# Kernel optimization log

Measured on AMD Instinct MI355X. Metric: run time of the kernel, lower is better.

## Reference

```python
import jax, jax.numpy as jnp
import numpy as np
from functools import partial

NUM_STEPS = 30  # Euler integration steps (inte_steps)


def _point_sample(vol, pts):
    """Trilinear sample of vol [C,D,H,W] at pts [N,3] (voxel coords, (d,h,w) order).
    Matches torch grid_sample(mode='bilinear', padding_mode='border', align_corners=True)
    after the normalize+flip done in PointPooling. Returns [C,N]."""
    dims = jnp.asarray(vol.shape[1:], dtype=pts.dtype)  # (D,H,W)
    p = jnp.clip(pts, 0.0, dims - 1.0)  # border padding == clamp coords
    p0 = jnp.floor(p)
    frac = p - p0  # [N,3]
    i0 = p0.astype(jnp.int32)
    i1 = jnp.minimum(i0 + 1, (dims - 1.0).astype(jnp.int32))
    d0, h0, w0 = i0[:, 0], i0[:, 1], i0[:, 2]
    d1, h1, w1 = i1[:, 0], i1[:, 1], i1[:, 2]
    fd, fh, fw = frac[:, 0], frac[:, 1], frac[:, 2]
    g = lambda d, h, w: vol[:, d, h, w]  # [C,N] gather
    c000, c001 = g(d0, h0, w0), g(d0, h0, w1)
    c010, c011 = g(d0, h1, w0), g(d0, h1, w1)
    c100, c101 = g(d1, h0, w0), g(d1, h0, w1)
    c110, c111 = g(d1, h1, w0), g(d1, h1, w1)
    c00 = c000 * (1 - fw) + c001 * fw
    c01 = c010 * (1 - fw) + c011 * fw
    c10 = c100 * (1 - fw) + c101 * fw
    c11 = c110 * (1 - fw) + c111 * fw
    c0 = c00 * (1 - fh) + c01 * fh
    c1 = c10 * (1 - fh) + c11 * fh
    return c0 * (1 - fd) + c1 * fd  # [C,N]


def _interp(flow, x):
    # flow [B,3,D,H,W], x [B,N,3] -> [B,N,3]
    out = jax.vmap(_point_sample)(flow, x)  # [B,3,N]
    return jnp.transpose(out, (0, 2, 1))


def _integrate_euler(flow, x, num_steps):
    flow = flow * (1.0 / num_steps)
    def step(x, _):
        return x + _interp(flow, x), None
    x, _ = jax.lax.scan(step, x, None, length=num_steps)
    return x


def _forward(verts, affine, flow_field):
    B, N, _ = verts.shape
    ones = jnp.ones((B, N, 1), dtype=verts.dtype)
    homog = jnp.concatenate([verts, ones], axis=-1)  # [B,N,4]
    pred = jnp.einsum('bij,bnj->bni', affine, homog)[..., :3]
    aux = _integrate_euler(flow_field, pred, NUM_STEPS)
    flow_int = aux - pred  # [B,N,3]
    pred = aux
    flow_int = jnp.transpose(flow_int, (0, 2, 1))[..., None, None]  # [B,3,N,1,1]
    homog2 = jnp.concatenate([pred, ones], axis=-1)
    inv_aff = jnp.linalg.inv(affine)
    pred = jnp.einsum('bij,bnj->bni', inv_aff, homog2)[..., :3]
    return pred, flow_int


def setup_inputs() -> dict:
    key = jax.random.key(0)
    k1, k2, k3 = jax.random.split(key, 3)
    B, N = 2, 140000
    D = H = W = 192
    dims = jnp.asarray([D - 1, H - 1, W - 1], dtype=jnp.float32)
    verts = jax.random.uniform(k1, (B, N, 3), dtype=jnp.float32) * dims
    affine = jnp.eye(4, dtype=jnp.float32)[None] + 0.01 * jax.random.normal(k2, (B, 4, 4), dtype=jnp.float32)
    flow_field = jax.random.normal(k3, (B, 3, D, H, W), dtype=jnp.float32)
    return {"verts": verts, "affine": affine, "flow_field": flow_field}


def reference(verts, affine, flow_field):
    return _forward(verts, affine, flow_field)
```

## Files before the change

kernel.cpp:

```cpp
#include <hip/hip_runtime.h>
#include <hip/hip_fp16.h>

#define NSTEPS 30
#define DIM 192
static constexpr long DHW = (long)DIM * DIM * DIM;
static constexpr int PTS_PER_WAVE = 21;

__global__ void invert4x4_kernel(const float* __restrict__ aff,
                                 float* __restrict__ out, int B) {
    int b = blockIdx.x * blockDim.x + threadIdx.x;
    if (b >= B) return;
    double a[16];
#pragma unroll
    for (int i = 0; i < 16; i++) a[i] = (double)aff[b * 16 + i];
    double s0 = a[0]*a[5]  - a[4]*a[1];
    double s1 = a[0]*a[6]  - a[4]*a[2];
    double s2 = a[0]*a[7]  - a[4]*a[3];
    double s3 = a[1]*a[6]  - a[5]*a[2];
    double s4 = a[1]*a[7]  - a[5]*a[3];
    double s5 = a[2]*a[7]  - a[6]*a[3];
    double c5 = a[10]*a[15] - a[14]*a[11];
    double c4 = a[9]*a[15]  - a[13]*a[11];
    double c3 = a[9]*a[14]  - a[13]*a[10];
    double c2 = a[8]*a[15]  - a[12]*a[11];
    double c1 = a[8]*a[14]  - a[12]*a[10];
    double c0 = a[8]*a[13]  - a[12]*a[9];
    double det = s0*c5 - s1*c4 + s2*c3 + s3*c2 - s4*c1 + s5*c0;
    double inv = 1.0 / det;
    double o[16];
    o[0]  = ( a[5]*c5 - a[6]*c4 + a[7]*c3) * inv;
    o[1]  = (-a[1]*c5 + a[2]*c4 - a[3]*c3) * inv;
    o[2]  = ( a[13]*s5 - a[14]*s4 + a[15]*s3) * inv;
    o[3]  = (-a[9]*s5 + a[10]*s4 - a[11]*s3) * inv;
    o[4]  = (-a[4]*c5 + a[6]*c2 - a[7]*c1) * inv;
    o[5]  = ( a[0]*c5 - a[2]*c2 + a[3]*c1) * inv;
    o[6]  = (-a[12]*s5 + a[14]*s2 - a[15]*s1) * inv;
    o[7]  = ( a[8]*s5 - a[10]*s2 + a[11]*s1) * inv;
    o[8]  = ( a[4]*c4 - a[5]*c2 + a[7]*c0) * inv;
    o[9]  = (-a[0]*c4 + a[1]*c2 - a[3]*c0) * inv;
    o[10] = ( a[12]*s4 - a[13]*s2 + a[15]*s0) * inv;
    o[11] = (-a[8]*s4 + a[9]*s2 - a[11]*s0) * inv;
    o[12] = (-a[4]*c3 + a[5]*c1 - a[6]*c0) * inv;
    o[13] = ( a[0]*c3 - a[1]*c1 + a[2]*c0) * inv;
    o[14] = (-a[12]*s3 + a[13]*s1 - a[14]*s0) * inv;
    o[15] = ( a[8]*s3 - a[9]*s1 + a[10]*s0) * inv;
#pragma unroll
    for (int i = 0; i < 16; i++) out[b * 16 + i] = (float)o[i];
}

__global__ __launch_bounds__(256) void repack_kernel(const float* __restrict__ flow,
                                                     __half* __restrict__ packed) {
    long vox = (long)blockIdx.x * blockDim.x + threadIdx.x;
    int b = blockIdx.y;
    if (vox >= DHW) return;
    const float* F = flow + (size_t)b * 3 * DHW;
    float f0 = F[vox];
    float f1 = F[vox + DHW];
    float f2 = F[vox + 2 * DHW];
    union { __half2 h2[2]; int2 i2; } u;
    u.h2[0] = __floats2half2_rn(f0, f1);
    u.h2[1] = __floats2half2_rn(f2, 0.0f);
    reinterpret_cast<int2*>(packed)[(size_t)b * DHW + vox] = u.i2;
}

__global__ __launch_bounds__(256) void deform_packed_kernel(
    const float* __restrict__ verts,
    const float* __restrict__ affine,
    const __half* __restrict__ packed,
    const float* __restrict__ invaff,
    float* __restrict__ out_pred,
    float* __restrict__ out_flow,
    int N, int B) {
    int lane = threadIdx.x & 63;
    int wib  = threadIdx.x >> 6;
    long gwave = (long)blockIdx.x * (blockDim.x >> 6) + wib;

    int piw = lane / 3;
    if (piw > PTS_PER_WAVE - 1) piw = PTS_PER_WAVE - 1;
    int ch = lane - piw * 3;
    if (ch > 2) ch = 2;

    long pt = gwave * PTS_PER_WAVE + piw;
    bool valid = (lane < 63) && (pt < (long)B * N);
    long ptc = valid ? pt : ((long)B * N - 1);
    int b = (int)(ptc / N);
    int n = (int)(ptc - (long)b * N);

    const float* A = affine + b * 16;
    const float* v = verts + (size_t)ptc * 3;
    float vx = v[0], vy = v[1], vz = v[2];
    float x = A[0] * vx + A[1] * vy + A[2]  * vz + A[3];
    float y = A[4] * vx + A[5] * vy + A[6]  * vz + A[7];
    float z = A[8] * vx + A[9] * vy + A[10] * vz + A[11];
    float p0 = (ch == 0) ? x : (ch == 1) ? y : z;

    const __half* Pb = packed + ((size_t)b * DHW) * 4 + ch;
    const float scale = (float)(1.0 / NSTEPS);

    float cc[8];
    int key = -1;
    int bl = piw * 3;

    for (int s = 0; s < NSTEPS; s++) {
        float pd = fminf(fmaxf(x, 0.0f), (float)(DIM - 1));
        float ph = fminf(fmaxf(y, 0.0f), (float)(DIM - 1));
        float pw = fminf(fmaxf(z, 0.0f), (float)(DIM - 1));
        float fd0 = floorf(pd), fh0 = floorf(ph), fw0 = floorf(pw);
        int d0 = (int)fd0, h0 = (int)fh0, w0 = (int)fw0;
        float fd = pd - fd0, fh = ph - fh0, fw = pw - fw0;

        int k = (d0 * DIM + h0) * DIM + w0;
        if (k != key) {
            key = k;
            int d1 = min(d0 + 1, DIM - 1);
            int h1 = min(h0 + 1, DIM - 1);
            int w1 = min(w0 + 1, DIM - 1);
            size_t r00 = (size_t)((d0 * DIM + h0) * DIM) * 4;
            size_t r01 = (size_t)((d0 * DIM + h1) * DIM) * 4;
            size_t r10 = (size_t)((d1 * DIM + h0) * DIM) * 4;
            size_t r11 = (size_t)((d1 * DIM + h1) * DIM) * 4;
            size_t o0 = (size_t)w0 * 4, o1 = (size_t)w1 * 4;
            cc[0] = __half2float(Pb[r00 + o0]) * scale;
            cc[1] = __half2float(Pb[r00 + o1]) * scale;
            cc[2] = __half2float(Pb[r01 + o0]) * scale;
            cc[3] = __half2float(Pb[r01 + o1]) * scale;
            cc[4] = __half2float(Pb[r10 + o0]) * scale;
            cc[5] = __half2float(Pb[r10 + o1]) * scale;
            cc[6] = __half2float(Pb[r11 + o0]) * scale;
            cc[7] = __half2float(Pb[r11 + o1]) * scale;
        }

        float omfw = 1.0f - fw, omfh = 1.0f - fh, omfd = 1.0f - fd;
        float c00 = cc[0] * omfw + cc[1] * fw;
        float c01 = cc[2] * omfw + cc[3] * fw;
        float c10 = cc[4] * omfw + cc[5] * fw;
        float c11 = cc[6] * omfw + cc[7] * fw;
        float c0 = c00 * omfh + c01 * fh;
        float c1 = c10 * omfh + c11 * fh;
        float val = c0 * omfd + c1 * fd;

        float v0 = __shfl(val, bl,     64);
        float v1 = __shfl(val, bl + 1, 64);
        float v2 = __shfl(val, bl + 2, 64);
        x += v0; y += v1; z += v2;
    }

    if (valid) {
        float posc = (ch == 0) ? x : (ch == 1) ? y : z;
        float fint = posc - p0;
        const float* Ai = invaff + b * 16 + ch * 4;
        float o = Ai[0] * x + Ai[1] * y + Ai[2] * z + Ai[3];
        out_pred[(size_t)ptc * 3 + ch] = o;
        out_flow[(size_t)b * 3 * N + (size_t)ch * N + n] = fint;
    }
}

__global__ __launch_bounds__(256) void deform_kernel(
    const float* __restrict__ verts,
    const float* __restrict__ affine,
    const float* __restrict__ flow,
    const float* __restrict__ invaff,
    float* __restrict__ out_pred,
    float* __restrict__ out_flow,
    int N, int B) {
    int lane = threadIdx.x & 63;
    int wib  = threadIdx.x >> 6;
    long gwave = (long)blockIdx.x * (blockDim.x >> 6) + wib;
    int piw = lane / 3;
    if (piw > PTS_PER_WAVE - 1) piw = PTS_PER_WAVE - 1;
    int ch = lane - piw * 3;
    if (ch > 2) ch = 2;
    long pt = gwave * PTS_PER_WAVE + piw;
    bool valid = (lane < 63) && (pt < (long)B * N);
    long ptc = valid ? pt : ((long)B * N - 1);
    int b = (int)(ptc / N);
    int n = (int)(ptc - (long)b * N);
    const float* A = affine + b * 16;
    const float* v = verts + (size_t)ptc * 3;
    float vx = v[0], vy = v[1], vz = v[2];
    float x = A[0] * vx + A[1] * vy + A[2]  * vz + A[3];
    float y = A[4] * vx + A[5] * vy + A[6]  * vz + A[7];
    float z = A[8] * vx + A[9] * vy + A[10] * vz + A[11];
    float p0 = (ch == 0) ? x : (ch == 1) ? y : z;
    const float* Fc = flow + ((size_t)b * 3 + ch) * (size_t)DHW;
    const float scale = (float)(1.0 / NSTEPS);
    float cc[8];
    int key = -1;
    int bl = piw * 3;
    for (int s = 0; s < NSTEPS; s++) {
        float pd = fminf(fmaxf(x, 0.0f), (float)(DIM - 1));
        float ph = fminf(fmaxf(y, 0.0f), (float)(DIM - 1));
        float pw = fminf(fmaxf(z, 0.0f), (float)(DIM - 1));
        float fd0 = floorf(pd), fh0 = floorf(ph), fw0 = floorf(pw);
        int d0 = (int)fd0, h0 = (int)fh0, w0 = (int)fw0;
        float fd = pd - fd0, fh = ph - fh0, fw = pw - fw0;
        int k = (d0 * DIM + h0) * DIM + w0;
        if (k != key) {
            key = k;
            int d1 = min(d0 + 1, DIM - 1);
            int h1 = min(h0 + 1, DIM - 1);
            int w1 = min(w0 + 1, DIM - 1);
            int r00 = (d0 * DIM + h0) * DIM;
            int r01 = (d0 * DIM + h1) * DIM;
            int r10 = (d1 * DIM + h0) * DIM;
            int r11 = (d1 * DIM + h1) * DIM;
            cc[0] = Fc[r00 + w0] * scale;
            cc[1] = Fc[r00 + w1] * scale;
            cc[2] = Fc[r01 + w0] * scale;
            cc[3] = Fc[r01 + w1] * scale;
            cc[4] = Fc[r10 + w0] * scale;
            cc[5] = Fc[r10 + w1] * scale;
            cc[6] = Fc[r11 + w0] * scale;
            cc[7] = Fc[r11 + w1] * scale;
        }
        float omfw = 1.0f - fw, omfh = 1.0f - fh, omfd = 1.0f - fd;
        float c00 = cc[0] * omfw + cc[1] * fw;
        float c01 = cc[2] * omfw + cc[3] * fw;
        float c10 = cc[4] * omfw + cc[5] * fw;
        float c11 = cc[6] * omfw + cc[7] * fw;
        float c0 = c00 * omfh + c01 * fh;
        float c1 = c10 * omfh + c11 * fh;
        float val = c0 * omfd + c1 * fd;
        float v0 = __shfl(val, bl,     64);
        float v1 = __shfl(val, bl + 1, 64);
        float v2 = __shfl(val, bl + 2, 64);
        x += v0; y += v1; z += v2;
    }
    if (valid) {
        float posc = (ch == 0) ? x : (ch == 1) ? y : z;
        float fint = posc - p0;
        const float* Ai = invaff + b * 16 + ch * 4;
        float o = Ai[0] * x + Ai[1] * y + Ai[2] * z + Ai[3];
        out_pred[(size_t)ptc * 3 + ch] = o;
        out_flow[(size_t)b * 3 * N + (size_t)ch * N + n] = fint;
    }
}

extern "C" void kernel_launch(void* const* d_in, const int* in_sizes, int n_in,
                              void* d_out, int out_size, void* d_ws, size_t ws_size,
                              hipStream_t stream) {
    const float* verts  = (const float*)d_in[0];
    const float* affine = (const float*)d_in[1];
    const float* flow   = (const float*)d_in[2];

    int B = in_sizes[1] / 16;
    int N = in_sizes[0] / (3 * B);

    float* out_pred = (float*)d_out;
    float* out_flow = out_pred + (size_t)B * N * 3;

    size_t packed_bytes = (size_t)B * DHW * 4 * sizeof(__half);
    bool use_packed = (ws_size >= packed_bytes + 256);

    long total_pts = (long)B * N;
    long waves  = (total_pts + PTS_PER_WAVE - 1) / PTS_PER_WAVE;
    long blocks = (waves + 3) / 4;

    if (use_packed) {
        __half* packed = (__half*)d_ws;
        float* invaff  = (float*)((char*)d_ws + packed_bytes);
        hipLaunchKernelGGL(invert4x4_kernel, dim3(1), dim3(64), 0, stream,
                           affine, invaff, B);
        long vblocks = (DHW + 255) / 256;
        hipLaunchKernelGGL(repack_kernel, dim3((unsigned)vblocks, B), dim3(256), 0,
                           stream, flow, packed);
        hipLaunchKernelGGL(deform_packed_kernel, dim3((unsigned)blocks), dim3(256),
                           0, stream, verts, affine, packed, invaff,
                           out_pred, out_flow, N, B);
    } else {
        float* invaff = (float*)d_ws;
        hipLaunchKernelGGL(invert4x4_kernel, dim3(1), dim3(64), 0, stream,
                           affine, invaff, B);
        hipLaunchKernelGGL(deform_kernel, dim3((unsigned)blocks), dim3(256), 0,
                           stream, verts, affine, flow, invaff,
                           out_pred, out_flow, N, B);
    }
}
```

Baseline: 306.0 us.

## Use one thread per point with packed half4 gathers and fused repack

Replaces the three-lanes-per-point deform kernel with one thread per point that loads all three flow channels from a single 8-byte packed voxel and does the trilinear blend itself, with no cross-lane shuffles. The repack kernel now handles four voxels per thread with float4 loads and 16-byte stores, folds the 1/NSTEPS scale into the packed data, and also does the 4x4 inverse, removing one launch. The aim is fewer gather instructions, no shuffles and better repack bandwidth. In exchange each thread holds more registers, and writes to the strided output are less coalesced.

```diff
diff --git a/kernel.cpp b/kernel.cpp
--- a/kernel.cpp
+++ b/kernel.cpp
@@ -6,10 +6,8 @@
 static constexpr long DHW = (long)DIM * DIM * DIM;
 static constexpr int PTS_PER_WAVE = 21;
 
-__global__ void invert4x4_kernel(const float* __restrict__ aff,
-                                 float* __restrict__ out, int B) {
-    int b = blockIdx.x * blockDim.x + threadIdx.x;
-    if (b >= B) return;
+__device__ __forceinline__ void invert4x4_one(const float* __restrict__ aff,
+                                              float* __restrict__ out, int b) {
     double a[16];
 #pragma unroll
     for (int i = 0; i < 16; i++) a[i] = (double)aff[b * 16 + i];
@@ -48,22 +46,43 @@
     for (int i = 0; i < 16; i++) out[b * 16 + i] = (float)o[i];
 }
 
-__global__ __launch_bounds__(256) void repack_kernel(const float* __restrict__ flow,
-                                                     __half* __restrict__ packed) {
-    long vox = (long)blockIdx.x * blockDim.x + threadIdx.x;
+__global__ void invert4x4_kernel(const float* __restrict__ aff,
+                                 float* __restrict__ out, int B) {
+    int b = blockIdx.x * blockDim.x + threadIdx.x;
+    if (b >= B) return;
+    invert4x4_one(aff, out, b);
+}
+
+__global__ __launch_bounds__(256) void repack4_kernel(
+    const float* __restrict__ flow, __half* __restrict__ packed,
+    const float* __restrict__ aff, float* __restrict__ invaff, int B) {
+    if (blockIdx.x == 0 && blockIdx.y == 0 && threadIdx.x < (unsigned)B)
+        invert4x4_one(aff, invaff, (int)threadIdx.x);
+
+    long vox = ((long)blockIdx.x * blockDim.x + threadIdx.x) * 4;
     int b = blockIdx.y;
     if (vox >= DHW) return;
     const float* F = flow + (size_t)b * 3 * DHW;
-    float f0 = F[vox];
-    float f1 = F[vox + DHW];
-    float f2 = F[vox + 2 * DHW];
-    union { __half2 h2[2]; int2 i2; } u;
-    u.h2[0] = __floats2half2_rn(f0, f1);
-    u.h2[1] = __floats2half2_rn(f2, 0.0f);
-    reinterpret_cast<int2*>(packed)[(size_t)b * DHW + vox] = u.i2;
-}
-
-__global__ __launch_bounds__(256) void deform_packed_kernel(
+    float4 f0 = *reinterpret_cast<const float4*>(F + vox);
+    float4 f1 = *reinterpret_cast<const float4*>(F + vox + DHW);
+    float4 f2 = *reinterpret_cast<const float4*>(F + vox + 2 * DHW);
+    const float s = (float)(1.0 / NSTEPS);
+    union { __half2 h2[4]; int4 i4; } u;
+    int4* dst = reinterpret_cast<int4*>(reinterpret_cast<int2*>(packed) +
+                                        (size_t)b * DHW + vox);
+    u.h2[0] = __floats2half2_rn(f0.x * s, f1.x * s);
+    u.h2[1] = __floats2half2_rn(f2.x * s, 0.0f);
+    u.h2[2] = __floats2half2_rn(f0.y * s, f1.y * s);
+    u.h2[3] = __floats2half2_rn(f2.y * s, 0.0f);
+    dst[0] = u.i4;
+    u.h2[0] = __floats2half2_rn(f0.z * s, f1.z * s);
+    u.h2[1] = __floats2half2_rn(f2.z * s, 0.0f);
+    u.h2[2] = __floats2half2_rn(f0.w * s, f1.w * s);
+    u.h2[3] = __floats2half2_rn(f2.w * s, 0.0f);
+    dst[1] = u.i4;
+}
+
+__global__ __launch_bounds__(256) void deform1_kernel(
     const float* __restrict__ verts,
     const float* __restrict__ affine,
     const __half* __restrict__ packed,
@@ -71,35 +90,31 @@
     float* __restrict__ out_pred,
     float* __restrict__ out_flow,
     int N, int B) {
-    int lane = threadIdx.x & 63;
-    int wib  = threadIdx.x >> 6;
-    long gwave = (long)blockIdx.x * (blockDim.x >> 6) + wib;
-
-    int piw = lane / 3;
-    if (piw > PTS_PER_WAVE - 1) piw = PTS_PER_WAVE - 1;
-    int ch = lane - piw * 3;
-    if (ch > 2) ch = 2;
-
-    long pt = gwave * PTS_PER_WAVE + piw;
-    bool valid = (lane < 63) && (pt < (long)B * N);
-    long ptc = valid ? pt : ((long)B * N - 1);
-    int b = (int)(ptc / N);
-    int n = (int)(ptc - (long)b * N);
+    int pt = blockIdx.x * blockDim.x + threadIdx.x;
+    int total = B * N;
+    if (pt >= total) return;
+    int b = pt / N;
+    int n = pt - b * N;
 
     const float* A = affine + b * 16;
-    const float* v = verts + (size_t)ptc * 3;
+    const float* v = verts + (size_t)pt * 3;
     float vx = v[0], vy = v[1], vz = v[2];
     float x = A[0] * vx + A[1] * vy + A[2]  * vz + A[3];
     float y = A[4] * vx + A[5] * vy + A[6]  * vz + A[7];
     float z = A[8] * vx + A[9] * vy + A[10] * vz + A[11];
-    float p0 = (ch == 0) ? x : (ch == 1) ? y : z;
-
-    const __half* Pb = packed + ((size_t)b * DHW) * 4 + ch;
-    const float scale = (float)(1.0 / NSTEPS);
-
-    float cc[8];
+    float x0 = x, y0 = y, z0 = z;
+
+    const int2* P = reinterpret_cast<const int2*>(packed) + (size_t)b * DHW;
+
+    float cx0, cx1, cx2, cx3, cx4, cx5, cx6, cx7;
+    float cy0, cy1, cy2, cy3, cy4, cy5, cy6, cy7;
+    float cz0, cz1, cz2, cz3, cz4, cz5, cz6, cz7;
+    cx0=cx1=cx2=cx3=cx4=cx5=cx6=cx7=0.f;
+    cy0=cy1=cy2=cy3=cy4=cy5=cy6=cy7=0.f;
+    cz0=cz1=cz2=cz3=cz4=cz5=cz6=cz7=0.f;
     int key = -1;
-    int bl = piw * 3;
+
+    union Cvt { int2 i2; __half2 h2[2]; };
 
     for (int s = 0; s < NSTEPS; s++) {
         float pd = fminf(fmaxf(x, 0.0f), (float)(DIM - 1));
@@ -109,50 +124,55 @@
         int d0 = (int)fd0, h0 = (int)fh0, w0 = (int)fw0;
         float fd = pd - fd0, fh = ph - fh0, fw = pw - fw0;
 
-        int k = (d0 * DIM + h0) * DIM + w0;
+        int r00 = (d0 * DIM + h0) * DIM;
+        int k = r00 + w0;
         if (k != key) {
             key = k;
             int d1 = min(d0 + 1, DIM - 1);
             int h1 = min(h0 + 1, DIM - 1);
             int w1 = min(w0 + 1, DIM - 1);
-            size_t r00 = (size_t)((d0 * DIM + h0) * DIM) * 4;
-            size_t r01 = (size_t)((d0 * DIM + h1) * DIM) * 4;
-            size_t r10 = (size_t)((d1 * DIM + h0) * DIM) * 4;
-            size_t r11 = (size_t)((d1 * DIM + h1) * DIM) * 4;
-            size_t o0 = (size_t)w0 * 4, o1 = (size_t)w1 * 4;
-            cc[0] = __half2float(Pb[r00 + o0]) * scale;
-            cc[1] = __half2float(Pb[r00 + o1]) * scale;
-            cc[2] = __half2float(Pb[r01 + o0]) * scale;
-            cc[3] = __half2float(Pb[r01 + o1]) * scale;
-            cc[4] = __half2float(Pb[r10 + o0]) * scale;
-            cc[5] = __half2float(Pb[r10 + o1]) * scale;
-            cc[6] = __half2float(Pb[r11 + o0]) * scale;
-            cc[7] = __half2float(Pb[r11 + o1]) * scale;
+            int r01 = (d0 * DIM + h1) * DIM;
+            int r10 = (d1 * DIM + h0) * DIM;
+            int r11 = (d1 * DIM + h1) * DIM;
+            int2 q0 = P[r00 + w0], q1 = P[r00 + w1];
+            int2 q2 = P[r01 + w0], q3 = P[r01 + w1];
+            int2 q4 = P[r10 + w0], q5 = P[r10 + w1];
+            int2 q6 = P[r11 + w0], q7 = P[r11 + w1];
+            Cvt u;
+            u.i2 = q0; cx0 = __low2float(u.h2[0]); cy0 = __high2float(u.h2[0]); cz0 = __low2float(u.h2[1]);
+            u.i2 = q1; cx1 = __low2float(u.h2[0]); cy1 = __high2float(u.h2[0]); cz1 = __low2float(u.h2[1]);
+            u.i2 = q2; cx2 = __low2float(u.h2[0]); cy2 = __high2float(u.h2[0]); cz2 = __low2float(u.h2[1]);
+            u.i2 = q3; cx3 = __low2float(u.h2[0]); cy3 = __high2float(u.h2[0]); cz3 = __low2float(u.h2[1]);
+            u.i2 = q4; cx4 = __low2float(u.h2[0]); cy4 = __high2float(u.h2[0]); cz4 = __low2float(u.h2[1]);
+            u.i2 = q5; cx5 = __low2float(u.h2[0]); cy5 = __high2float(u.h2[0]); cz5 = __low2float(u.h2[1]);
+            u.i2 = q6; cx6 = __low2float(u.h2[0]); cy6 = __high2float(u.h2[0]); cz6 = __low2float(u.h2[1]);
+            u.i2 = q7; cx7 = __low2float(u.h2[0]); cy7 = __high2float(u.h2[0]); cz7 = __low2float(u.h2[1]);
         }
 
-        float omfw = 1.0f - fw, omfh = 1.0f - fh, omfd = 1.0f - fd;
-        float c00 = cc[0] * omfw + cc[1] * fw;
-        float c01 = cc[2] * omfw + cc[3] * fw;
-        float c10 = cc[4] * omfw + cc[5] * fw;
-        float c11 = cc[6] * omfw + cc[7] * fw;
-        float c0 = c00 * omfh + c01 * fh;
-        float c1 = c10 * omfh + c11 * fh;
-        float val = c0 * omfd + c1 * fd;
-
-        float v0 = __shfl(val, bl,     64);
-        float v1 = __shfl(val, bl + 1, 64);
-        float v2 = __shfl(val, bl + 2, 64);
-        x += v0; y += v1; z += v2;
-    }
-
-    if (valid) {
-        float posc = (ch == 0) ? x : (ch == 1) ? y : z;
-        float fint = posc - p0;
-        const float* Ai = invaff + b * 16 + ch * 4;
-        float o = Ai[0] * x + Ai[1] * y + Ai[2] * z + Ai[3];
-        out_pred[(size_t)ptc * 3 + ch] = o;
-        out_flow[(size_t)b * 3 * N + (size_t)ch * N + n] = fint;
-    }
+        float wd0 = 1.0f - fd, wh0 = 1.0f - fh, ww0 = 1.0f - fw;
+        float a00 = wd0 * wh0, a01 = wd0 * fh, a10 = fd * wh0, a11 = fd * fh;
+        float t0 = a00 * ww0, t1 = a00 * fw;
+        float t2 = a01 * ww0, t3 = a01 * fw;
+        float t4 = a10 * ww0, t5 = a10 * fw;
+        float t6 = a11 * ww0, t7 = a11 * fw;
+        x += t0*cx0 + t1*cx1 + t2*cx2 + t3*cx3 + t4*cx4 + t5*cx5 + t6*cx6 + t7*cx7;
+        y += t0*cy0 + t1*cy1 + t2*cy2 + t3*cy3 + t4*cy4 + t5*cy5 + t6*cy6 + t7*cy7;
+        z += t0*cz0 + t1*cz1 + t2*cz2 + t3*cz3 + t4*cz4 + t5*cz5 + t6*cz6 + t7*cz7;
+    }
+
+    float fx = x - x0, fy = y - y0, fz = z - z0;
+    const float* Ai = invaff + b * 16;
+    float ox = Ai[0] * x + Ai[1] * y + Ai[2]  * z + Ai[3];
+    float oy = Ai[4] * x + Ai[5] * y + Ai[6]  * z + Ai[7];
+    float oz = Ai[8] * x + Ai[9] * y + Ai[10] * z + Ai[11];
+    size_t po = (size_t)pt * 3;
+    out_pred[po + 0] = ox;
+    out_pred[po + 1] = oy;
+    out_pred[po + 2] = oz;
+    size_t fb = (size_t)b * 3 * N + n;
+    out_flow[fb]             = fx;
+    out_flow[fb + (size_t)N] = fy;
+    out_flow[fb + 2 * (size_t)N] = fz;
 }
 
 __global__ __launch_bounds__(256) void deform_kernel(
@@ -252,23 +272,22 @@
     size_t packed_bytes = (size_t)B * DHW * 4 * sizeof(__half);
     bool use_packed = (ws_size >= packed_bytes + 256);
 
-    long total_pts = (long)B * N;
-    long waves  = (total_pts + PTS_PER_WAVE - 1) / PTS_PER_WAVE;
-    long blocks = (waves + 3) / 4;
-
     if (use_packed) {
         __half* packed = (__half*)d_ws;
         float* invaff  = (float*)((char*)d_ws + packed_bytes);
-        hipLaunchKernelGGL(invert4x4_kernel, dim3(1), dim3(64), 0, stream,
-                           affine, invaff, B);
-        long vblocks = (DHW + 255) / 256;
-        hipLaunchKernelGGL(repack_kernel, dim3((unsigned)vblocks, B), dim3(256), 0,
-                           stream, flow, packed);
-        hipLaunchKernelGGL(deform_packed_kernel, dim3((unsigned)blocks), dim3(256),
+        long vblocks = (DHW / 4 + 255) / 256;
+        hipLaunchKernelGGL(repack4_kernel, dim3((unsigned)vblocks, B), dim3(256),
+                           0, stream, flow, packed, affine, invaff, B);
+        int total = B * N;
+        int blocks = (total + 255) / 256;
+        hipLaunchKernelGGL(deform1_kernel, dim3((unsigned)blocks), dim3(256),
                            0, stream, verts, affine, packed, invaff,
                            out_pred, out_flow, N, B);
     } else {
         float* invaff = (float*)d_ws;
+        long total_pts = (long)B * N;
+        long waves  = (total_pts + PTS_PER_WAVE - 1) / PTS_PER_WAVE;
+        long blocks = (waves + 3) / 4;
         hipLaunchKernelGGL(invert4x4_kernel, dim3(1), dim3(64), 0, stream,
                            affine, invaff, B);
         hipLaunchKernelGGL(deform_kernel, dim3((unsigned)blocks), dim3(256), 0,
```

Result: slower. 316.0 us (+3.3%).

## Bin points by depth slice and drop fp16 flow repack

Applied to the files above, without the earlier changes.

Replaces the per-call fp16 repack of the whole flow field with direct fp32 gathers from the original planar layout. Adds a counting sort of points by batch and initial depth slice (histogram, scan, scatter) so that neighbouring waves sample nearby regions of the volume, which should improve cache locality. The repack pass, which read and wrote the full volume, is removed. In exchange there are four extra small kernels, including a single-threaded serial scan, and each gather becomes three separate fp32 loads per corner from three planes instead of one packed load.

```diff
diff --git a/kernel.cpp b/kernel.cpp
--- a/kernel.cpp
+++ b/kernel.cpp
@@ -1,15 +1,13 @@
 #include <hip/hip_runtime.h>
-#include <hip/hip_fp16.h>
 
 #define NSTEPS 30
 #define DIM 192
 static constexpr long DHW = (long)DIM * DIM * DIM;
 static constexpr int PTS_PER_WAVE = 21;
-
-__global__ void invert4x4_kernel(const float* __restrict__ aff,
-                                 float* __restrict__ out, int B) {
-    int b = blockIdx.x * blockDim.x + threadIdx.x;
-    if (b >= B) return;
+static constexpr int MAX_LDS_BINS = 2048;
+
+__device__ __forceinline__ void invert4x4_one(const float* __restrict__ aff,
+                                              float* __restrict__ out, int b) {
     double a[16];
 #pragma unroll
     for (int i = 0; i < 16; i++) a[i] = (double)aff[b * 16 + i];
@@ -48,26 +46,86 @@
     for (int i = 0; i < 16; i++) out[b * 16 + i] = (float)o[i];
 }
 
-__global__ __launch_bounds__(256) void repack_kernel(const float* __restrict__ flow,
-                                                     __half* __restrict__ packed) {
-    long vox = (long)blockIdx.x * blockDim.x + threadIdx.x;
-    int b = blockIdx.y;
-    if (vox >= DHW) return;
-    const float* F = flow + (size_t)b * 3 * DHW;
-    float f0 = F[vox];
-    float f1 = F[vox + DHW];
-    float f2 = F[vox + 2 * DHW];
-    union { __half2 h2[2]; int2 i2; } u;
-    u.h2[0] = __floats2half2_rn(f0, f1);
-    u.h2[1] = __floats2half2_rn(f2, 0.0f);
-    reinterpret_cast<int2*>(packed)[(size_t)b * DHW + vox] = u.i2;
-}
-
-__global__ __launch_bounds__(256) void deform_packed_kernel(
+__device__ __forceinline__ int bin_of_point(const float* __restrict__ verts,
+                                            const float* __restrict__ affine,
+                                            int pt, int N) {
+    int b = pt / N;
+    const float* A = affine + b * 16;
+    const float* v = verts + (size_t)pt * 3;
+    float x = A[0] * v[0] + A[1] * v[1] + A[2] * v[2] + A[3];
+    int d = (int)x;
+    d = min(max(d, 0), DIM - 1);
+    return b * DIM + d;
+}
+
+__global__ void setup_kernel(const float* __restrict__ aff,
+                             float* __restrict__ invaff,
+                             int* __restrict__ hist, int NB, int B) {
+    for (int i = threadIdx.x; i < NB; i += blockDim.x) hist[i] = 0;
+    if (threadIdx.x < (unsigned)B) invert4x4_one(aff, invaff, (int)threadIdx.x);
+}
+
+__global__ __launch_bounds__(256) void hist_kernel(
+    const float* __restrict__ verts, const float* __restrict__ affine,
+    int* __restrict__ hist, int N, int B, int total) {
+    __shared__ int lh[MAX_LDS_BINS];
+    int NB = B * DIM;
+    bool use_lds = (NB <= MAX_LDS_BINS);
+    if (use_lds) {
+        for (int i = threadIdx.x; i < NB; i += blockDim.x) lh[i] = 0;
+        __syncthreads();
+    }
+    int stride = gridDim.x * blockDim.x;
+    for (int pt = blockIdx.x * blockDim.x + threadIdx.x; pt < total; pt += stride) {
+        int bin = bin_of_point(verts, affine, pt, N);
+        if (use_lds) atomicAdd(&lh[bin], 1);
+        else         atomicAdd(&hist[bin], 1);
+    }
+    if (use_lds) {
+        __syncthreads();
+        for (int i = threadIdx.x; i < NB; i += blockDim.x) {
+            int c = lh[i];
+            if (c) atomicAdd(&hist[i], c);
+        }
+    }
+}
+
+__global__ void scan_kernel(const int* __restrict__ hist,
+                            int* __restrict__ cursors, int NB) {
+    __shared__ int lh[MAX_LDS_BINS];
+    if (NB <= MAX_LDS_BINS) {
+        for (int i = threadIdx.x; i < NB; i += blockDim.x) lh[i] = hist[i];
+        __syncthreads();
+        if (threadIdx.x == 0) {
+            int acc = 0;
+            for (int i = 0; i < NB; i++) { int c = lh[i]; lh[i] = acc; acc += c; }
+        }
+        __syncthreads();
+        for (int i = threadIdx.x; i < NB; i += blockDim.x) cursors[i] = lh[i];
+    } else if (threadIdx.x == 0) {
+        int acc = 0;
+        for (int i = 0; i < NB; i++) { int c = hist[i]; cursors[i] = acc; acc += c; }
+    }
+}
+
+__global__ __launch_bounds__(256) void scatter_kernel(
+    const float* __restrict__ verts, const float* __restrict__ affine,
+    int* __restrict__ cursors, int* __restrict__ order,
+    int N, int B, int total) {
+    int stride = gridDim.x * blockDim.x;
+    for (int pt = blockIdx.x * blockDim.x + threadIdx.x; pt < total; pt += stride) {
+        int bin = bin_of_point(verts, affine, pt, N);
+        int idx = atomicAdd(&cursors[bin], 1);
+        order[idx] = pt;
+    }
+}
+
+__global__ __launch_bounds__(256) void deform_sorted_kernel(
     const float* __restrict__ verts,
     const float* __restrict__ affine,
-    const __half* __restrict__ packed,
+    const float* __restrict__ flow,
     const float* __restrict__ invaff,
+    const int*   __restrict__ order,
     float* __restrict__ out_pred,
     float* __restrict__ out_flow,
     int N, int B) {
@@ -80,9 +138,11 @@
     int ch = lane - piw * 3;
     if (ch > 2) ch = 2;
 
-    long pt = gwave * PTS_PER_WAVE + piw;
-    bool valid = (lane < 63) && (pt < (long)B * N);
-    long ptc = valid ? pt : ((long)B * N - 1);
+    long total = (long)B * N;
+    long slot = gwave * PTS_PER_WAVE + piw;
+    bool valid = (lane < 63) && (slot < total);
+    long slotc = valid ? slot : (total - 1);
+    long ptc = (long)min(max(order[slotc], 0), (int)(total - 1));
     int b = (int)(ptc / N);
     int n = (int)(ptc - (long)b * N);
 
@@ -94,7 +154,7 @@
     float z = A[8] * vx + A[9] * vy + A[10] * vz + A[11];
     float p0 = (ch == 0) ? x : (ch == 1) ? y : z;
 
-    const __half* Pb = packed + ((size_t)b * DHW) * 4 + ch;
+    const float* Fc = flow + ((size_t)b * 3 + ch) * (size_t)DHW;
     const float scale = (float)(1.0 / NSTEPS);
 
     float cc[8];
@@ -115,19 +175,18 @@
             int d1 = min(d0 + 1, DIM - 1);
             int h1 = min(h0 + 1, DIM - 1);
             int w1 = min(w0 + 1, DIM - 1);
-            size_t r00 = (size_t)((d0 * DIM + h0) * DIM) * 4;
-            size_t r01 = (size_t)((d0 * DIM + h1) * DIM) * 4;
-            size_t r10 = (size_t)((d1 * DIM + h0) * DIM) * 4;
-            size_t r11 = (size_t)((d1 * DIM + h1) * DIM) * 4;
-            size_t o0 = (size_t)w0 * 4, o1 = (size_t)w1 * 4;
-            cc[0] = __half2float(Pb[r00 + o0]) * scale;
-            cc[1] = __half2float(Pb[r00 + o1]) * scale;
-            cc[2] = __half2float(Pb[r01 + o0]) * scale;
-            cc[3] = __half2float(Pb[r01 + o1]) * scale;
-            cc[4] = __half2float(Pb[r10 + o0]) * scale;
-            cc[5] = __half2float(Pb[r10 + o1]) * scale;
-            cc[6] = __half2float(Pb[r11 + o0]) * scale;
-            cc[7] = __half2float(Pb[r11 + o1]) * scale;
+            int r00 = (d0 * DIM + h0) * DIM;
+            int r01 = (d0 * DIM + h1) * DIM;
+            int r10 = (d1 * DIM + h0) * DIM;
+            int r11 = (d1 * DIM + h1) * DIM;
+            cc[0] = Fc[r00 + w0] * scale;
+            cc[1] = Fc[r00 + w1] * scale;
+            cc[2] = Fc[r01 + w0] * scale;
+            cc[3] = Fc[r01 + w1] * scale;
+            cc[4] = Fc[r10 + w0] * scale;
+            cc[5] = Fc[r10 + w1] * scale;
+            cc[6] = Fc[r11 + w0] * scale;
+            cc[7] = Fc[r11 + w1] * scale;
         }
 
         float omfw = 1.0f - fw, omfh = 1.0f - fh, omfd = 1.0f - fd;
@@ -245,32 +304,46 @@
 
     int B = in_sizes[1] / 16;
     int N = in_sizes[0] / (3 * B);
+    int total = B * N;
+    int NB = B * DIM;
 
     float* out_pred = (float*)d_out;
     float* out_flow = out_pred + (size_t)B * N * 3;
 
-    size_t packed_bytes = (size_t)B * DHW * 4 * sizeof(__half);
-    bool use_packed = (ws_size >= packed_bytes + 256);
-
-    long total_pts = (long)B * N;
-    long waves  = (total_pts + PTS_PER_WAVE - 1) / PTS_PER_WAVE;
+    size_t off_inv  = 0;
+    size_t off_hist = (off_inv + (size_t)B * 16 * 4 + 15) & ~(size_t)15;
+    size_t off_cur  = (off_hist + (size_t)NB * 4 + 15) & ~(size_t)15;
+    size_t off_ord  = (off_cur + (size_t)NB * 4 + 15) & ~(size_t)15;
+    size_t need     = off_ord + (size_t)total * 4;
+    bool use_sorted = (ws_size >= need);
+
+    long waves  = ((long)total + PTS_PER_WAVE - 1) / PTS_PER_WAVE;
     long blocks = (waves + 3) / 4;
 
-    if (use_packed) {
-        __half* packed = (__half*)d_ws;
-        float* invaff  = (float*)((char*)d_ws + packed_bytes);
-        hipLaunchKernelGGL(invert4x4_kernel, dim3(1), dim3(64), 0, stream,
-                           affine, invaff, B);
-        long vblocks = (DHW + 255) / 256;
-        hipLaunchKernelGGL(repack_kernel, dim3((unsigned)vblocks, B), dim3(256), 0,
-                           stream, flow, packed);
-        hipLaunchKernelGGL(deform_packed_kernel, dim3((unsigned)blocks), dim3(256),
-                           0, stream, verts, affine, packed, invaff,
+    if (use_sorted) {
+        float* invaff = (float*)((char*)d_ws + off_inv);
+        int* hist     = (int*)((char*)d_ws + off_hist);
+        int* cursors  = (int*)((char*)d_ws + off_cur);
+        int* order    = (int*)((char*)d_ws + off_ord);
+
+        int sblocks = (total + 255) / 256;
+        if (sblocks > 1024) sblocks = 1024;
+
+        hipLaunchKernelGGL(setup_kernel, dim3(1), dim3(256), 0, stream,
+                           affine, invaff, hist, NB, B);
+        hipLaunchKernelGGL(hist_kernel, dim3(sblocks), dim3(256), 0, stream,
+                           verts, affine, hist, N, B, total);
+        hipLaunchKernelGGL(scan_kernel, dim3(1), dim3(256), 0, stream,
+                           hist, cursors, NB);
+        hipLaunchKernelGGL(scatter_kernel, dim3(sblocks), dim3(256), 0, stream,
+                           verts, affine, cursors, order, N, B, total);
+        hipLaunchKernelGGL(deform_sorted_kernel, dim3((unsigned)blocks), dim3(256),
+                           0, stream, verts, affine, flow, invaff, order,
                            out_pred, out_flow, N, B);
     } else {
         float* invaff = (float*)d_ws;
-        hipLaunchKernelGGL(invert4x4_kernel, dim3(1), dim3(64), 0, stream,
-                           affine, invaff, B);
+        hipLaunchKernelGGL(setup_kernel, dim3(1), dim3(256), 0, stream,
+                           affine, invaff, (int*)((char*)d_ws + 256), 0, B);
         hipLaunchKernelGGL(deform_kernel, dim3((unsigned)blocks), dim3(256), 0,
                            stream, verts, affine, flow, invaff,
                            out_pred, out_flow, N, B);
```

Result: slower. 470.1 us (+53.6%).

## Switch packed flow to planar fp16 per channel with vectorized repack

Applied to the files above, without the earlier changes.

Changes the fp16 flow copy from an interleaved 4-half-per-voxel layout to three planar channel arrays, and repacks two voxels per thread with float2 loads and half2 stores. This drops the padding channel, so the repack writes less, and index math becomes 32-bit. In exchange, the three lanes that sample one point now gather from three separate planes instead of one shared 8-byte chunk. That can multiply the cache lines touched per trilinear sample.

```diff
diff --git a/kernel.cpp b/kernel.cpp
--- a/kernel.cpp
+++ b/kernel.cpp
@@ -48,19 +48,20 @@
     for (int i = 0; i < 16; i++) out[b * 16 + i] = (float)o[i];
 }
 
-__global__ __launch_bounds__(256) void repack_kernel(const float* __restrict__ flow,
-                                                     __half* __restrict__ packed) {
-    long vox = (long)blockIdx.x * blockDim.x + threadIdx.x;
+__global__ __launch_bounds__(256) void repack_kernel(
+    const float* __restrict__ flow, __half* __restrict__ packed) {
+    long vox2 = (long)blockIdx.x * blockDim.x + threadIdx.x;
     int b = blockIdx.y;
-    if (vox >= DHW) return;
+    if (vox2 >= DHW / 2) return;
+    long vox = vox2 * 2;
     const float* F = flow + (size_t)b * 3 * DHW;
-    float f0 = F[vox];
-    float f1 = F[vox + DHW];
-    float f2 = F[vox + 2 * DHW];
-    union { __half2 h2[2]; int2 i2; } u;
-    u.h2[0] = __floats2half2_rn(f0, f1);
-    u.h2[1] = __floats2half2_rn(f2, 0.0f);
-    reinterpret_cast<int2*>(packed)[(size_t)b * DHW + vox] = u.i2;
+    __half* P = packed + (size_t)b * 3 * DHW;
+#pragma unroll
+    for (int c = 0; c < 3; c++) {
+        float2 f = *reinterpret_cast<const float2*>(F + (size_t)c * DHW + vox);
+        *reinterpret_cast<__half2*>(P + (size_t)c * DHW + vox) =
+            __floats2half2_rn(f.x, f.y);
+    }
 }
 
 __global__ __launch_bounds__(256) void deform_packed_kernel(
@@ -94,7 +95,7 @@
     float z = A[8] * vx + A[9] * vy + A[10] * vz + A[11];
     float p0 = (ch == 0) ? x : (ch == 1) ? y : z;
 
-    const __half* Pb = packed + ((size_t)b * DHW) * 4 + ch;
+    const __half* Pb = packed + ((size_t)b * 3 + ch) * (size_t)DHW;
     const float scale = (float)(1.0 / NSTEPS);
 
     float cc[8];
@@ -115,19 +116,18 @@
             int d1 = min(d0 + 1, DIM - 1);
             int h1 = min(h0 + 1, DIM - 1);
             int w1 = min(w0 + 1, DIM - 1);
-            size_t r00 = (size_t)((d0 * DIM + h0) * DIM) * 4;
-            size_t r01 = (size_t)((d0 * DIM + h1) * DIM) * 4;
-            size_t r10 = (size_t)((d1 * DIM + h0) * DIM) * 4;
-            size_t r11 = (size_t)((d1 * DIM + h1) * DIM) * 4;
-            size_t o0 = (size_t)w0 * 4, o1 = (size_t)w1 * 4;
-            cc[0] = __half2float(Pb[r00 + o0]) * scale;
-            cc[1] = __half2float(Pb[r00 + o1]) * scale;
-            cc[2] = __half2float(Pb[r01 + o0]) * scale;
-            cc[3] = __half2float(Pb[r01 + o1]) * scale;
-            cc[4] = __half2float(Pb[r10 + o0]) * scale;
-            cc[5] = __half2float(Pb[r10 + o1]) * scale;
-            cc[6] = __half2float(Pb[r11 + o0]) * scale;
-            cc[7] = __half2float(Pb[r11 + o1]) * scale;
+            int r00 = (d0 * DIM + h0) * DIM;
+            int r01 = (d0 * DIM + h1) * DIM;
+            int r10 = (d1 * DIM + h0) * DIM;
+            int r11 = (d1 * DIM + h1) * DIM;
+            cc[0] = __half2float(Pb[r00 + w0]) * scale;
+            cc[1] = __half2float(Pb[r00 + w1]) * scale;
+            cc[2] = __half2float(Pb[r01 + w0]) * scale;
+            cc[3] = __half2float(Pb[r01 + w1]) * scale;
+            cc[4] = __half2float(Pb[r10 + w0]) * scale;
+            cc[5] = __half2float(Pb[r10 + w1]) * scale;
+            cc[6] = __half2float(Pb[r11 + w0]) * scale;
+            cc[7] = __half2float(Pb[r11 + w1]) * scale;
         }
 
         float omfw = 1.0f - fw, omfh = 1.0f - fh, omfd = 1.0f - fd;
@@ -249,7 +249,7 @@
     float* out_pred = (float*)d_out;
     float* out_flow = out_pred + (size_t)B * N * 3;
 
-    size_t packed_bytes = (size_t)B * DHW * 4 * sizeof(__half);
+    size_t packed_bytes = (size_t)B * 3 * DHW * sizeof(__half);
     bool use_packed = (ws_size >= packed_bytes + 256);
 
     long total_pts = (long)B * N;
@@ -261,7 +261,7 @@
         float* invaff  = (float*)((char*)d_ws + packed_bytes);
         hipLaunchKernelGGL(invert4x4_kernel, dim3(1), dim3(64), 0, stream,
                            affine, invaff, B);
-        long vblocks = (DHW + 255) / 256;
+        long vblocks = (DHW / 2 + 255) / 256;
         hipLaunchKernelGGL(repack_kernel, dim3((unsigned)vblocks, B), dim3(256), 0,
                            stream, flow, packed);
         hipLaunchKernelGGL(deform_packed_kernel, dim3((unsigned)blocks), dim3(256),
```

New measurement: 367.1 us. 1.2x slower.
